# Kernel tuning notes

Measured on AMD Instinct MI355X. Metric: run time of the kernel, lower is better.

The kernel has to match this reference:

```python
import jax, jax.numpy as jnp
import numpy as np

B, T, D, H = 4, 2048, 1024, 16
HD = D // H  # head_dim = 64


def setup_inputs() -> dict:
    key = jax.random.key(0)
    k1, k2, k3 = jax.random.split(key, 3)
    scale_in = 1.0 / np.sqrt(D)
    return {
        "x": jax.random.normal(k1, (B, T, D), dtype=jnp.float32),
        "w_attn": jax.random.normal(k2, (D, 3 * D), dtype=jnp.float32) * scale_in,
        "b_attn": jnp.zeros((3 * D,), dtype=jnp.float32),
        "w_proj": jax.random.normal(k3, (D, D), dtype=jnp.float32) * scale_in,
        "b_proj": jnp.zeros((D,), dtype=jnp.float32),
    }


def reference(x, w_attn, b_attn, w_proj, b_proj):
    Bv, Tv, Dv = x.shape
    qkv = x @ w_attn + b_attn  # (B,T,3D)
    q, k, v = jnp.split(qkv, 3, axis=-1)
    # (B,T,D) -> (B,H,T,hd)
    q = q.reshape(Bv, Tv, H, HD).transpose(0, 2, 1, 3)
    k = k.reshape(Bv, Tv, H, HD).transpose(0, 2, 1, 3)
    v = v.reshape(Bv, Tv, H, HD).transpose(0, 2, 1, 3)
    scale = 1.0 / np.sqrt(HD)
    scores = jnp.einsum("bhqd,bhkd->bhqk", q, k) * scale  # (B,H,T,T)
    causal = jnp.tril(jnp.ones((Tv, Tv), dtype=bool))
    scores = jnp.where(causal, scores, jnp.finfo(scores.dtype).min)
    attn = jax.nn.softmax(scores, axis=-1)
    y = jnp.einsum("bhqk,bhkd->bhqd", attn, v)  # (B,H,T,hd)
    y = y.transpose(0, 2, 1, 3).reshape(Bv, Tv, Dv)
    return y @ w_proj + b_proj
```

## Files before the change

### kernel.cpp

```cpp
#include <hip/hip_runtime.h>
#include <math.h>

typedef __bf16 bf16_t;
typedef __attribute__((ext_vector_type(8))) __bf16 bf16x8;
typedef __attribute__((ext_vector_type(4))) float f32x4;

#define B_  4
#define T_  2048
#define D_  1024
#define H_  16
#define HD_ 64
#define D3_ 3072

__device__ __forceinline__ void load_lds16(const bf16_t* g, char* lds) {
  __builtin_amdgcn_global_load_lds(
      (const __attribute__((address_space(1))) void*)g,
      (__attribute__((address_space(3))) void*)lds, 16, 0, 0);
}

__global__ __launch_bounds__(256) void convert_bf16(
    const float* __restrict__ in, bf16_t* __restrict__ out, int n4) {
  int idx = blockIdx.x * 256 + threadIdx.x;
  int stride = gridDim.x * 256;
  for (int i = idx; i < n4; i += stride) {
    float4 v = ((const float4*)in)[i];
    alignas(8) bf16_t o4[4] = {(bf16_t)v.x, (bf16_t)v.y, (bf16_t)v.z, (bf16_t)v.w};
    ((uint2*)out)[i] = *(const uint2*)o4;
  }
}

__global__ __launch_bounds__(256) void transpose_convert(
    const float* __restrict__ W, bf16_t* __restrict__ Wt, int K, int N) {
  __shared__ float tile[64][65];
  const int k0 = blockIdx.x * 64, n0 = blockIdx.y * 64;
  const int tid = threadIdx.x;
  const int r = tid >> 4, c4 = (tid & 15) * 4;
#pragma unroll
  for (int i = 0; i < 4; ++i) {
    float4 v = *(const float4*)(W + (size_t)(k0 + r + i * 16) * N + n0 + c4);
    tile[r + i * 16][c4 + 0] = v.x;
    tile[r + i * 16][c4 + 1] = v.y;
    tile[r + i * 16][c4 + 2] = v.z;
    tile[r + i * 16][c4 + 3] = v.w;
  }
  __syncthreads();
#pragma unroll
  for (int i = 0; i < 4; ++i) {
    int n = r + i * 16;
    alignas(8) bf16_t o4[4];
#pragma unroll
    for (int j = 0; j < 4; ++j) o4[j] = (bf16_t)tile[c4 + j][n];
    *(uint2*)(Wt + (size_t)(n0 + n) * K + k0 + c4) = *(const uint2*)o4;
  }
}

#define GBM 128
#define GBN 128
#define GBK 32

template <bool BF16_OUT>
__global__ __launch_bounds__(256) void gemm_bt_mfma(
    const bf16_t* __restrict__ A, const bf16_t* __restrict__ Bt,
    const float* __restrict__ bias, void* __restrict__ Cv,
    int M, int N, int K) {
  __shared__ __align__(16) bf16_t Asl[2][GBM * GBK];
  __shared__ __align__(16) bf16_t Bsl[2][GBN * GBK];

  const int tid = threadIdx.x;
  const int w = tid >> 6, l = tid & 63;
  const int l15 = l & 15, lhi = l >> 4;
  const int row0 = blockIdx.y * GBM, col0 = blockIdx.x * GBN;
  const int wr = (w >> 1) * 64, wc = (w & 1) * 64;

  const int srow = tid >> 2;
  const int sf = (srow & 3) ^ ((srow >> 2) & 3);
  const int slog = (tid & 3) ^ sf;
  const int rf = (l15 & 3) ^ ((l15 >> 2) & 3);
  const int rchunk = lhi ^ rf;

  f32x4 acc[4][4];
#pragma unroll
  for (int i = 0; i < 4; ++i)
#pragma unroll
    for (int j = 0; j < 4; ++j) acc[i][j] = (f32x4){0.f, 0.f, 0.f, 0.f};

  const bf16_t* Abase = A + (size_t)row0 * K;
  const bf16_t* Bbase = Bt + (size_t)col0 * K;

  auto stage = [&](int buf, int k0) {
#pragma unroll
    for (int issue = 0; issue < 2; ++issue) {
      const bf16_t* ga = Abase + (size_t)(issue * 64 + srow) * K + k0 + slog * 8;
      load_lds16(ga, (char*)&Asl[buf][0] + issue * 4096 + w * 1024);
      const bf16_t* gb = Bbase + (size_t)(issue * 64 + srow) * K + k0 + slog * 8;
      load_lds16(gb, (char*)&Bsl[buf][0] + issue * 4096 + w * 1024);
    }
  };

  const int nt = K / GBK;
  stage(0, 0);

  for (int t = 0; t < nt; ++t) {
    __syncthreads();
    if (t + 1 < nt) stage((t + 1) & 1, (t + 1) * GBK);

    const bf16_t* As = &Asl[t & 1][0];
    const bf16_t* Bs = &Bsl[t & 1][0];
    bf16x8 af[4], bf[4];
#pragma unroll
    for (int i = 0; i < 4; ++i)
      af[i] = *(const bf16x8*)&As[(wr + i * 16 + l15) * GBK + rchunk * 8];
#pragma unroll
    for (int j = 0; j < 4; ++j)
      bf[j] = *(const bf16x8*)&Bs[(wc + j * 16 + l15) * GBK + rchunk * 8];
#pragma unroll
    for (int i = 0; i < 4; ++i)
#pragma unroll
      for (int j = 0; j < 4; ++j)
        acc[i][j] =
            __builtin_amdgcn_mfma_f32_16x16x32_bf16(af[i], bf[j], acc[i][j], 0, 0, 0);
  }

#pragma unroll
  for (int j = 0; j < 4; ++j) {
    int colr = col0 + wc + j * 16 + l15;
    float bv = bias[colr];
#pragma unroll
    for (int i = 0; i < 4; ++i) {
#pragma unroll
      for (int r = 0; r < 4; ++r) {
        int rowr = row0 + wr + i * 16 + lhi * 4 + r;
        float val = acc[i][j][r] + bv;
        if constexpr (BF16_OUT)
          ((bf16_t*)Cv)[(size_t)rowr * N + colr] = (bf16_t)val;
        else
          ((float*)Cv)[(size_t)rowr * N + colr] = val;
      }
    }
  }
}

__global__ __launch_bounds__(256) void transpose_v(
    const bf16_t* __restrict__ qkv, bf16_t* __restrict__ Vg) {
  const int bh = blockIdx.y;
  const int b = bh >> 4, h = bh & 15;
  const int t0 = blockIdx.x * 64;
  const int tid = threadIdx.x;
  const int d = tid & 63;
  const int w = tid >> 6;
  alignas(16) bf16_t tmp[16];
#pragma unroll
  for (int j = 0; j < 16; ++j) {
    int t = t0 + w * 16 + j;
    tmp[j] = qkv[(size_t)(b * T_ + t) * D3_ + 2 * D_ + h * HD_ + d];
  }
  bf16_t* dst = Vg + (size_t)(bh * HD_ + d) * T_ + t0 + w * 16;
  *(uint4*)(dst) = *(const uint4*)(tmp);
  *(uint4*)(dst + 8) = *(const uint4*)(tmp + 8);
}

#define QBLK 128
#define KBLK 64

__global__ __launch_bounds__(256, 4) void attn_fwd_mfma(
    const bf16_t* __restrict__ qkv, const bf16_t* __restrict__ Vg,
    bf16_t* __restrict__ y) {
  const int lin = blockIdx.x;
  const int bh = (lin & 7) * 8 + ((lin >> 3) & 7);
  const int qt = (T_ / QBLK - 1) - (lin >> 6);
  const int b = bh >> 4, h = bh & 15;
  const int Q0 = qt * QBLK;
  const int tid = threadIdx.x;
  const int w = tid >> 6, l = tid & 63;
  const int l15 = l & 15, lhi = l >> 4;

  __shared__ __align__(16) bf16_t K_lds[2][KBLK * 64];
  __shared__ __align__(16) bf16_t V_lds[KBLK * 64];
  __shared__ __align__(16) bf16_t P_lds[4][16][72];

  const int sr = tid >> 3, sp = tid & 7;
  const int slc = sp ^ (sr & 7);
  const int swz = (l15 & 7);

  auto stageK = [&](int buf, int kt) {
    const bf16_t* src =
        qkv + (size_t)(b * T_ + kt * KBLK + sr) * D3_ + D_ + h * HD_ + slc * 8;
    char* dst = (char*)(&K_lds[buf][0]) + w * 1024;
    load_lds16(src, dst);
    load_lds16(src + (size_t)32 * D3_, dst + 4096);
  };
  auto stageV = [&](int kt) {
    const bf16_t* src = Vg + ((size_t)bh * HD_ + sr) * T_ + kt * KBLK + slc * 8;
    char* dst = (char*)(&V_lds[0]) + w * 1024;
    load_lds16(src, dst);
    load_lds16(src + (size_t)32 * T_, dst + 4096);
  };

  bf16x8 qf[2][2];
#pragma unroll
  for (int g = 0; g < 2; ++g) {
    int q = Q0 + w * 32 + g * 16 + l15;
#pragma unroll
    for (int c = 0; c < 2; ++c) {
      const bf16_t* p = qkv + (size_t)(b * T_ + q) * D3_ + h * HD_ + c * 32 + lhi * 8;
      bf16x8 v = *(const bf16x8*)p;
#pragma unroll
      for (int e = 0; e < 8; ++e) v[e] = (bf16_t)((float)v[e] * 0.125f);
      qf[g][c] = v;
    }
  }

  f32x4 accO[2][4];
#pragma unroll
  for (int g = 0; g < 2; ++g)
#pragma unroll
    for (int dg = 0; dg < 4; ++dg) accO[g][dg] = (f32x4){0.f, 0.f, 0.f, 0.f};
  float m[2] = {-INFINITY, -INFINITY};
  float lsum[2] = {0.f, 0.f};

  const int ntiles = Q0 / KBLK + 2;
  const int qg0 = Q0 + w * 32;
  const int qg1 = qg0 + 16;

  stageK(0, 0);
  __syncthreads();

  for (int kt = 0; kt < ntiles; ++kt) {
    const int cur = kt & 1;
    const int ktb = kt * KBLK;
    stageV(kt);
    if (kt + 1 < ntiles) stageK(cur ^ 1, kt + 1);

    const bool act0 = (ktb <= qg0 + 15);
    const bool act1 = (ktb <= qg1 + 15);
    uint2 pp1[4];

#pragma unroll
    for (int g = 0; g < 2; ++g) {
      if (!(g == 0 ? act0 : act1)) continue;
      const int qg = g == 0 ? qg0 : qg1;

      f32x4 s[4];
#pragma unroll
      for (int n = 0; n < 4; ++n) s[n] = (f32x4){0.f, 0.f, 0.f, 0.f};
#pragma unroll
      for (int c = 0; c < 2; ++c) {
#pragma unroll
        for (int n = 0; n < 4; ++n) {
          bf16x8 kf = *(const bf16x8*)&K_lds[cur][(n * 16 + l15) * 64 +
                                                 (((c * 4 + lhi) ^ swz) * 8)];
          s[n] = __builtin_amdgcn_mfma_f32_16x16x32_bf16(kf, qf[g][c], s[n], 0, 0, 0);
        }
      }

      float sv[4][4];
#pragma unroll
      for (int n = 0; n < 4; ++n)
#pragma unroll
        for (int r = 0; r < 4; ++r) sv[n][r] = s[n][r];
      if (ktb + KBLK - 1 > qg) {
        const int qml = qg + l15 - ktb - lhi * 4;
#pragma unroll
        for (int n = 0; n < 4; ++n)
#pragma unroll
          for (int r = 0; r < 4; ++r)
            if (n * 16 + r > qml) sv[n][r] = -INFINITY;
      }

      float pm = sv[0][0];
#pragma unroll
      for (int n = 0; n < 4; ++n)
#pragma unroll
        for (int r = 0; r < 4; ++r) pm = fmaxf(pm, sv[n][r]);
      pm = fmaxf(pm, __shfl_xor(pm, 16));
      pm = fmaxf(pm, __shfl_xor(pm, 32));

      if (!__all(pm <= m[g] + 8.f)) {
        float mn = fmaxf(m[g], pm);
        float corrq = __expf(m[g] - mn);
        m[g] = mn;
        lsum[g] *= corrq;
        float cr[4];
#pragma unroll
        for (int r = 0; r < 4; ++r) cr[r] = __shfl(corrq, lhi * 4 + r);
#pragma unroll
        for (int dg = 0; dg < 4; ++dg)
#pragma unroll
          for (int r = 0; r < 4; ++r) accO[g][dg][r] *= cr[r];
      }
      const float mn = m[g];

      float rowsum = 0.f;
#pragma unroll
      for (int n = 0; n < 4; ++n) {
        alignas(8) bf16_t p4[4];
#pragma unroll
        for (int r = 0; r < 4; ++r) {
          float p = __expf(sv[n][r] - mn);
          rowsum += p;
          p4[r] = (bf16_t)p;
        }
        if (g == 0)
          *(uint2*)&P_lds[w][l15][n * 16 + lhi * 4] = *(const uint2*)p4;
        else
          pp1[n] = *(const uint2*)p4;
      }
      rowsum += __shfl_xor(rowsum, 16);
      rowsum += __shfl_xor(rowsum, 32);
      lsum[g] += rowsum;
    }

    __syncthreads();

    if (act0) {
#pragma unroll
      for (int c2 = 0; c2 < 2; ++c2) {
        bf16x8 pf = *(const bf16x8*)&P_lds[w][l15][c2 * 32 + lhi * 8];
#pragma unroll
        for (int dg = 0; dg < 4; ++dg) {
          bf16x8 vf = *(const bf16x8*)&V_lds[(dg * 16 + l15) * 64 +
                                             (((c2 * 4 + lhi) ^ swz) * 8)];
          accO[0][dg] =
              __builtin_amdgcn_mfma_f32_16x16x32_bf16(pf, vf, accO[0][dg], 0, 0, 0);
        }
      }
    }
    if (act1) {
#pragma unroll
      for (int n = 0; n < 4; ++n)
        *(uint2*)&P_lds[w][l15][n * 16 + lhi * 4] = pp1[n];
#pragma unroll
      for (int c2 = 0; c2 < 2; ++c2) {
        bf16x8 pf = *(const bf16x8*)&P_lds[w][l15][c2 * 32 + lhi * 8];
#pragma unroll
        for (int dg = 0; dg < 4; ++dg) {
          bf16x8 vf = *(const bf16x8*)&V_lds[(dg * 16 + l15) * 64 +
                                             (((c2 * 4 + lhi) ^ swz) * 8)];
          accO[1][dg] =
              __builtin_amdgcn_mfma_f32_16x16x32_bf16(pf, vf, accO[1][dg], 0, 0, 0);
        }
      }
    }

    __syncthreads();
  }

#pragma unroll
  for (int g = 0; g < 2; ++g)
#pragma unroll
    for (int r = 0; r < 4; ++r) {
      float ls = __shfl(lsum[g], lhi * 4 + r);
      float inv = 1.f / ls;
      int q = Q0 + w * 32 + g * 16 + lhi * 4 + r;
      bf16_t* yr = y + (size_t)(b * T_ + q) * D_ + h * HD_ + l15;
#pragma unroll
      for (int dg = 0; dg < 4; ++dg) yr[dg * 16] = (bf16_t)(accO[g][dg][r] * inv);
    }
}

extern "C" void kernel_launch(void* const* d_in, const int* in_sizes, int n_in,
                              void* d_out, int out_size, void* d_ws, size_t ws_size,
                              hipStream_t stream) {
  const float* x      = (const float*)d_in[0];
  const float* w_attn = (const float*)d_in[1];
  const float* b_attn = (const float*)d_in[2];
  const float* w_proj = (const float*)d_in[3];
  const float* b_proj = (const float*)d_in[4];
  float* out = (float*)d_out;

  const int M = B_ * T_;

  bf16_t* xb      = (bf16_t*)d_ws;
  bf16_t* wattnT  = xb + (size_t)M * D_;
  bf16_t* wprojT  = wattnT + (size_t)D3_ * D_;
  bf16_t* qkv_bf  = wprojT + (size_t)D_ * D_;
  bf16_t* Vg      = qkv_bf + (size_t)M * D3_;
  bf16_t* y_bf    = xb;

  convert_bf16<<<2048, 256, 0, stream>>>(x, xb, M * D_ / 4);
  transpose_convert<<<dim3(D_ / 64, D3_ / 64), 256, 0, stream>>>(w_attn, wattnT, D_, D3_);
  transpose_convert<<<dim3(D_ / 64, D_ / 64), 256, 0, stream>>>(w_proj, wprojT, D_, D_);
  gemm_bt_mfma<true><<<dim3(D3_ / GBN, M / GBM), 256, 0, stream>>>(
      xb, wattnT, b_attn, qkv_bf, M, D3_, D_);
  transpose_v<<<dim3(T_ / 64, B_ * H_), 256, 0, stream>>>(qkv_bf, Vg);
  attn_fwd_mfma<<<dim3(T_ / QBLK * B_ * H_), 256, 0, stream>>>(qkv_bf, Vg, y_bf);
  gemm_bt_mfma<false><<<dim3(D_ / GBN, M / GBM), 256, 0, stream>>>(
      y_bf, wprojT, b_proj, out, M, D_, D_);
}
```

Before: 190.3 us.

## Triple-buffer GEMM loads, raise MFMA priority, defer attention row-sum reduction

The GEMM moves from double to triple LDS buffering, with two tiles prefetched ahead and a partial vmcnt wait in place of a full __syncthreads, so global loads overlap compute more deeply. MFMA sections in the GEMM and attention kernels are wrapped in s_setprio to favour matrix issue across waves. The attention softmax row-sum shuffles move out of the per-tile loop and run once in the epilogue, and the score copy array is dropped. This costs extra LDS per GEMM block, which may lower occupancy, and the last iterations issue redundant clamped loads.

```diff
diff --git a/kernel.cpp b/kernel.cpp
--- a/kernel.cpp
+++ b/kernel.cpp
@@ -63,8 +63,8 @@
     const bf16_t* __restrict__ A, const bf16_t* __restrict__ Bt,
     const float* __restrict__ bias, void* __restrict__ Cv,
     int M, int N, int K) {
-  __shared__ __align__(16) bf16_t Asl[2][GBM * GBK];
-  __shared__ __align__(16) bf16_t Bsl[2][GBN * GBK];
+  __shared__ __align__(16) bf16_t Asl[3][GBM * GBK];
+  __shared__ __align__(16) bf16_t Bsl[3][GBN * GBK];
 
   const int tid = threadIdx.x;
   const int w = tid >> 6, l = tid & 63;
@@ -99,13 +99,16 @@
 
   const int nt = K / GBK;
   stage(0, 0);
+  stage(1, GBK);
 
   for (int t = 0; t < nt; ++t) {
-    __syncthreads();
-    if (t + 1 < nt) stage((t + 1) & 1, (t + 1) * GBK);
-
-    const bf16_t* As = &Asl[t & 1][0];
-    const bf16_t* Bs = &Bsl[t & 1][0];
+    asm volatile("s_waitcnt vmcnt(4)" ::: "memory");
+    __builtin_amdgcn_s_barrier();
+    const int t2 = (t + 2 < nt) ? t + 2 : nt - 1;
+    stage((t + 2) % 3, t2 * GBK);
+
+    const bf16_t* As = &Asl[t % 3][0];
+    const bf16_t* Bs = &Bsl[t % 3][0];
     bf16x8 af[4], bf[4];
 #pragma unroll
     for (int i = 0; i < 4; ++i)
@@ -113,12 +116,14 @@
 #pragma unroll
     for (int j = 0; j < 4; ++j)
       bf[j] = *(const bf16x8*)&Bs[(wc + j * 16 + l15) * GBK + rchunk * 8];
+    __builtin_amdgcn_s_setprio(1);
 #pragma unroll
     for (int i = 0; i < 4; ++i)
 #pragma unroll
       for (int j = 0; j < 4; ++j)
         acc[i][j] =
             __builtin_amdgcn_mfma_f32_16x16x32_bf16(af[i], bf[j], acc[i][j], 0, 0, 0);
+    __builtin_amdgcn_s_setprio(0);
   }
 
 #pragma unroll
@@ -243,6 +248,7 @@
       f32x4 s[4];
 #pragma unroll
       for (int n = 0; n < 4; ++n) s[n] = (f32x4){0.f, 0.f, 0.f, 0.f};
+      __builtin_amdgcn_s_setprio(1);
 #pragma unroll
       for (int c = 0; c < 2; ++c) {
 #pragma unroll
@@ -252,26 +258,22 @@
           s[n] = __builtin_amdgcn_mfma_f32_16x16x32_bf16(kf, qf[g][c], s[n], 0, 0, 0);
         }
       }
-
-      float sv[4][4];
-#pragma unroll
-      for (int n = 0; n < 4; ++n)
-#pragma unroll
-        for (int r = 0; r < 4; ++r) sv[n][r] = s[n][r];
+      __builtin_amdgcn_s_setprio(0);
+
       if (ktb + KBLK - 1 > qg) {
         const int qml = qg + l15 - ktb - lhi * 4;
 #pragma unroll
         for (int n = 0; n < 4; ++n)
 #pragma unroll
           for (int r = 0; r < 4; ++r)
-            if (n * 16 + r > qml) sv[n][r] = -INFINITY;
-      }
-
-      float pm = sv[0][0];
+            if (n * 16 + r > qml) s[n][r] = -INFINITY;
+      }
+
+      float pm = s[0][0];
 #pragma unroll
       for (int n = 0; n < 4; ++n)
 #pragma unroll
-        for (int r = 0; r < 4; ++r) pm = fmaxf(pm, sv[n][r]);
+        for (int r = 0; r < 4; ++r) pm = fmaxf(pm, s[n][r]);
       pm = fmaxf(pm, __shfl_xor(pm, 16));
       pm = fmaxf(pm, __shfl_xor(pm, 32));
 
@@ -296,7 +298,7 @@
         alignas(8) bf16_t p4[4];
 #pragma unroll
         for (int r = 0; r < 4; ++r) {
-          float p = __expf(sv[n][r] - mn);
+          float p = __expf(s[n][r] - mn);
           rowsum += p;
           p4[r] = (bf16_t)p;
         }
@@ -305,14 +307,13 @@
         else
           pp1[n] = *(const uint2*)p4;
       }
-      rowsum += __shfl_xor(rowsum, 16);
-      rowsum += __shfl_xor(rowsum, 32);
       lsum[g] += rowsum;
     }
 
     __syncthreads();
 
     if (act0) {
+      __builtin_amdgcn_s_setprio(1);
 #pragma unroll
       for (int c2 = 0; c2 < 2; ++c2) {
         bf16x8 pf = *(const bf16x8*)&P_lds[w][l15][c2 * 32 + lhi * 8];
@@ -324,11 +325,13 @@
               __builtin_amdgcn_mfma_f32_16x16x32_bf16(pf, vf, accO[0][dg], 0, 0, 0);
         }
       }
+      __builtin_amdgcn_s_setprio(0);
     }
     if (act1) {
 #pragma unroll
       for (int n = 0; n < 4; ++n)
         *(uint2*)&P_lds[w][l15][n * 16 + lhi * 4] = pp1[n];
+      __builtin_amdgcn_s_setprio(1);
 #pragma unroll
       for (int c2 = 0; c2 < 2; ++c2) {
         bf16x8 pf = *(const bf16x8*)&P_lds[w][l15][c2 * 32 + lhi * 8];
@@ -340,22 +343,27 @@
               __builtin_amdgcn_mfma_f32_16x16x32_bf16(pf, vf, accO[1][dg], 0, 0, 0);
         }
       }
+      __builtin_amdgcn_s_setprio(0);
     }
 
     __syncthreads();
   }
 
 #pragma unroll
-  for (int g = 0; g < 2; ++g)
+  for (int g = 0; g < 2; ++g) {
+    float ls = lsum[g];
+    ls += __shfl_xor(ls, 16);
+    ls += __shfl_xor(ls, 32);
 #pragma unroll
     for (int r = 0; r < 4; ++r) {
-      float ls = __shfl(lsum[g], lhi * 4 + r);
-      float inv = 1.f / ls;
+      float lr = __shfl(ls, lhi * 4 + r);
+      float inv = 1.f / lr;
       int q = Q0 + w * 32 + g * 16 + lhi * 4 + r;
       bf16_t* yr = y + (size_t)(b * T_ + q) * D_ + h * HD_ + l15;
 #pragma unroll
       for (int dg = 0; dg < 4; ++dg) yr[dg * 16] = (bf16_t)(accO[g][dg][r] * inv);
     }
+  }
 }
 
 extern "C" void kernel_launch(void* const* d_in, const int* in_sizes, int n_in,
```

After: 194.0 us. Within noise of the previous version (+2.0%).
